# Kernel tuning notes

Measured on AMD Instinct MI355X. Metric: run time of the kernel, lower is better.

The kernel has to match this reference:

```python
import jax, jax.numpy as jnp
import numpy as np
import math

ALPHA = 1.3
N_ITER = 50


def entmax_bisect(logits, alpha=ALPHA, n_iter=N_ITER):
    # logits: [..., D]; entmax over the last axis via bisection on tau.
    x = logits / max(1.0, abs(alpha - 1.0))  # divisor is 1.0 for alpha=1.3
    x = x - jnp.max(x, axis=-1, keepdims=True)  # max_x subtraction (differentiable, as in torch)
    xs = jax.lax.stop_gradient(x)  # tau_lo/tau_hi are .detach()'d in the original
    tau_lo = jnp.min(xs, axis=-1, keepdims=True) - 1.0
    tau_hi = jnp.max(xs, axis=-1, keepdims=True) - 1e-6
    inv = 1.0 / (alpha - 1.0)

    def body(_, carry):
        lo, hi = carry
        tau = (lo + hi) * 0.5
        p = jnp.maximum(xs - tau, 0.0) ** inv
        f = jnp.sum(p, axis=-1, keepdims=True) ** (alpha - 1.0)
        big = f > 1.0
        return (jnp.where(big, tau, lo), jnp.where(big, hi, tau))

    tau_lo, tau_hi = jax.lax.fori_loop(0, n_iter, body, (tau_lo, tau_hi))
    tau = (tau_lo + tau_hi) * 0.5
    p = jnp.maximum(x - tau, 0.0) ** inv
    return p / (jnp.sum(p, axis=-1, keepdims=True) + 1e-12)


def setup_inputs() -> dict:
    key = jax.random.key(0)
    kq, kk, kv = jax.random.split(key, 3)
    B, N, D = 16, 2048, 64
    return {
        "q": jax.random.normal(kq, (B, N, D), dtype=jnp.float32),
        "k": jax.random.normal(kk, (B, N, D), dtype=jnp.float32),
        "v": jax.random.normal(kv, (B, N, D), dtype=jnp.float32),
    }


def reference(q, k, v):
    d = q.shape[-1]
    scores = jnp.einsum("bnd,bmd->bnm", q, k) / math.sqrt(d)  # [B,N,N]
    attn = entmax_bisect(scores, alpha=ALPHA)
    out = jnp.einsum("bnm,bmd->bnd", attn, v)
    return out, attn
```

## Files before the change

kernel.cpp:

```cpp
#include <hip/hip_runtime.h>


#define NBATCH 16
#define NSEQ   2048
#define DHEAD  64
#define OUT_OFF (NBATCH * NSEQ * DHEAD)
#define INV_A    3.3333333f
#define INV_A_M1 2.3333333f
#define IDXM 0x7FFu
#define VALM 0xFFFFF800u

typedef float  vfloat4 __attribute__((ext_vector_type(4)));
typedef float  f32x4   __attribute__((ext_vector_type(4)));
typedef short  bf16x8  __attribute__((ext_vector_type(8)));
typedef unsigned short u16x8 __attribute__((ext_vector_type(8)));

__device__ __forceinline__ float fast_log2(float x) { return __builtin_amdgcn_logf(x); }
__device__ __forceinline__ float fast_exp2(float x) { return __builtin_amdgcn_exp2f(x); }

__device__ __forceinline__ unsigned bf16_rne(float x) {
    const unsigned u = __float_as_uint(x);
    return (u + 0x7FFFu + ((u >> 16) & 1u)) >> 16;
}

__global__ __launch_bounds__(256) void ksplit_kernel(
    const float* __restrict__ K, unsigned short* __restrict__ Khi,
    unsigned short* __restrict__ Klo)
{
    const size_t idx = (size_t)blockIdx.x * 256 + threadIdx.x;
    const float4 x = ((const float4*)K)[idx];
    const float xs[4] = {x.x, x.y, x.z, x.w};
    unsigned short h[4], l[4];
    #pragma unroll
    for (int i = 0; i < 4; ++i) {
        const unsigned hr = bf16_rne(xs[i]);
        h[i] = (unsigned short)hr;
        l[i] = (unsigned short)bf16_rne(xs[i] - __uint_as_float(hr << 16));
    }
    ((ushort4*)Khi)[idx] = make_ushort4(h[0], h[1], h[2], h[3]);
    ((ushort4*)Klo)[idx] = make_ushort4(l[0], l[1], l[2], l[3]);
}

__global__ __launch_bounds__(512) void entmax_attn_kernel(
    const float* __restrict__ Q, const float* __restrict__ V,
    float* __restrict__ Out,
    const unsigned short* __restrict__ Khi, const unsigned short* __restrict__ Klo)
{
    __shared__ __align__(16) float reg0[8192];
    __shared__ __align__(16) float cpk[8 * 256];

    const int tid  = threadIdx.x;
    const int w    = tid >> 6;
    const int lane = tid & 63;
    const int arow = lane & 15;
    const int lg   = lane >> 4;

    const int i   = blockIdx.x;
    const int xcd = i & 7;
    const int j2  = i >> 3;
    const int b   = xcd + 8 * (j2 & 1);
    const int rb  = j2 >> 1;
    const int n0  = rb * 16;

    const float* Vb = V + (size_t)b * NSEQ * DHEAD;
    const unsigned short* KhiB = Khi + (size_t)b * NSEQ * DHEAD;
    const unsigned short* KloB = Klo + (size_t)b * NSEQ * DHEAD;
    char* ldsHi = (char*)reg0;
    char* ldsLo = (char*)reg0 + 16384;

    bf16x8 a_hi[2], a_lo[2];
    {
        const float* qrow = Q + ((size_t)b * NSEQ + (size_t)(n0 + arow)) * DHEAD;
        #pragma unroll
        for (int ks = 0; ks < 2; ++ks) {
            const int d0 = ks * 32 + lg * 8;
            const float4 x0 = *(const float4*)(qrow + d0);
            const float4 x1 = *(const float4*)(qrow + d0 + 4);
            const float xs[8] = {x0.x, x0.y, x0.z, x0.w, x1.x, x1.y, x1.z, x1.w};
            #pragma unroll
            for (int e = 0; e < 8; ++e) {
                const float xq = xs[e] * 0.125f;
                const unsigned hr = bf16_rne(xq);
                a_hi[ks][e] = (short)hr;
                a_lo[ks][e] = (short)bf16_rne(xq - __uint_as_float(hr << 16));
            }
        }
    }

    float s[2][32];
    const int kap = 16 * w + arow;

    const int keyA = tid >> 3, cA = tid & 7;
    const int keyB = keyA + 64;
    const size_t gA = (size_t)keyA * DHEAD + cA * 8;
    const size_t gB = (size_t)keyB * DHEAD + cA * 8;
    const int ofA = keyA * 128 + ((cA ^ (keyA & 7)) << 4);
    const int ofB = keyB * 128 + ((cA ^ (keyA & 7)) << 4);

    u16x8 shA = *(const u16x8*)(KhiB + gA), slA = *(const u16x8*)(KloB + gA);
    u16x8 shB = *(const u16x8*)(KhiB + gB), slB = *(const u16x8*)(KloB + gB);

    #pragma unroll
    for (int g = 0; g < 4; ++g) {
        f32x4 acc[4];
        #pragma unroll
        for (int tt = 0; tt < 4; ++tt) acc[tt] = (f32x4){0.f, 0.f, 0.f, 0.f};

        #pragma unroll
        for (int tt = 0; tt < 4; ++tt) {
            const int t = 4 * g + tt;
            __syncthreads();
            *(u16x8*)(ldsHi + ofA) = shA;  *(u16x8*)(ldsLo + ofA) = slA;
            *(u16x8*)(ldsHi + ofB) = shB;  *(u16x8*)(ldsLo + ofB) = slB;
            __syncthreads();

            #pragma unroll
            for (int ks = 0; ks < 2; ++ks) {
                const int loff = kap * 128 + ((((ks << 2) | lg) ^ (kap & 7)) << 4);
                const bf16x8 bh = *(const bf16x8*)(ldsHi + loff);
                const bf16x8 bl = *(const bf16x8*)(ldsLo + loff);
                acc[tt] = __builtin_amdgcn_mfma_f32_16x16x32_bf16(a_hi[ks], bh, acc[tt], 0, 0, 0);
                acc[tt] = __builtin_amdgcn_mfma_f32_16x16x32_bf16(a_hi[ks], bl, acc[tt], 0, 0, 0);
                acc[tt] = __builtin_amdgcn_mfma_f32_16x16x32_bf16(a_lo[ks], bh, acc[tt], 0, 0, 0);
            }
            if (t < 15) {
                const size_t tb = (size_t)(t + 1) * (128 * DHEAD);
                shA = *(const u16x8*)(KhiB + tb + gA);
                slA = *(const u16x8*)(KloB + tb + gA);
                shB = *(const u16x8*)(KhiB + tb + gB);
                slB = *(const u16x8*)(KloB + tb + gB);
            }
        }

        __syncthreads();
        #pragma unroll
        for (int tt = 0; tt < 4; ++tt)
            #pragma unroll
            for (int i2 = 0; i2 < 4; ++i2)
                reg0[(lg * 4 + i2) * 512 + tt * 128 + kap] = acc[tt][i2];
        __syncthreads();
        #pragma unroll
        for (int r = 0; r < 2; ++r)
            #pragma unroll
            for (int jj = 0; jj < 8; ++jj)
                s[r][8 * g + jj] = reg0[(2 * w + r) * 512 + jj * 64 + lane];
    }
    __syncthreads();

    unsigned* pk0 = (unsigned*)(cpk + w * 256);
    unsigned* pk1 = pk0 + 128;
    float* prow = reg0 + w * 1024;
    const unsigned long long lt_mask = (1ull << lane) - 1ull;
    const int na = n0 + 2 * w;

    float mx0 = s[0][0], mx1 = s[1][0];
    #pragma unroll
    for (int j = 1; j < 32; ++j) { mx0 = fmaxf(mx0, s[0][j]); mx1 = fmaxf(mx1, s[1][j]); }
    #pragma unroll
    for (int off = 32; off >= 1; off >>= 1) {
        mx0 = fmaxf(mx0, __shfl_xor(mx0, off, 64));
        mx1 = fmaxf(mx1, __shfl_xor(mx1, off, 64));
    }

    int base0 = 0, base1 = 0;
    #pragma unroll
    for (int j = 0; j < 32; ++j) {
        const float v0 = s[0][j] - mx0;
        const float v1 = s[1][j] - mx1;
        const bool a0 = v0 > -1.0f;
        const bool a1 = v1 > -1.0f;
        const unsigned long long bm0 = __ballot(a0);
        const unsigned long long bm1 = __ballot(a1);
        const int q0 = base0 + __popcll(bm0 & lt_mask);
        const int q1 = base1 + __popcll(bm1 & lt_mask);
        const unsigned idx = (unsigned)(j * 64 + lane);
        if (a0 && q0 < 128) pk0[q0] = (__float_as_uint(v0) & VALM) | idx;
        if (a1 && q1 < 128) pk1[q1] = (__float_as_uint(v1) & VALM) | idx;
        base0 += __popcll(bm0);
        base1 += __popcll(bm1);
    }
    const int A0 = base0, A1 = base1;

    float* arow0 = Out + OUT_OFF + ((size_t)b * NSEQ + na) * NSEQ;
    float* arow1 = arow0 + NSEQ;

    if (A0 <= 128 && A1 <= 128) {
        const unsigned u00 = pk0[lane],      u01 = pk0[64 + lane];
        const unsigned u10 = pk1[lane],      u11 = pk1[64 + lane];
        const float cv00 = __uint_as_float(u00 & VALM);
        const float cv01 = __uint_as_float(u01 & VALM);
        const float cv10 = __uint_as_float(u10 & VALM);
        const float cv11 = __uint_as_float(u11 & VALM);
        const bool ok00 = lane < A0, ok01 = 64 + lane < A0;
        const bool ok10 = lane < A1, ok11 = 64 + lane < A1;

        float lo0 = -1.0f, hi0 = -1e-6f, lo1 = -1.0f, hi1 = -1e-6f;
        #pragma unroll 1
        for (int it = 0; it < 8; ++it) {
            const float ta = 0.5f * (lo0 + hi0);
            const float tb = 0.5f * (lo1 + hi1);
            const float t00 = cv00 - ta, t01 = cv01 - ta;
            const float t10 = cv10 - tb, t11 = cv11 - tb;
            float S0 = ((ok00 && t00 > 0.f) ? fast_exp2(INV_A * fast_log2(t00)) : 0.f)
                     + ((ok01 && t01 > 0.f) ? fast_exp2(INV_A * fast_log2(t01)) : 0.f);
            float S1 = ((ok10 && t10 > 0.f) ? fast_exp2(INV_A * fast_log2(t10)) : 0.f)
                     + ((ok11 && t11 > 0.f) ? fast_exp2(INV_A * fast_log2(t11)) : 0.f);
            #pragma unroll
            for (int off = 32; off >= 1; off >>= 1) {
                S0 += __shfl_xor(S0, off, 64);
                S1 += __shfl_xor(S1, off, 64);
            }
            if (S0 > 1.f) lo0 = ta; else hi0 = ta;
            if (S1 > 1.f) lo1 = tb; else hi1 = tb;
        }
        float tau0 = lo0, tau1 = lo1;
        #pragma unroll 1
        for (int it = 0; it < 2; ++it) {
            const float t00 = cv00 - tau0, t01 = cv01 - tau0;
            const float t10 = cv10 - tau1, t11 = cv11 - tau1;
            float Sa0 = 0.f, Sb0 = 0.f, Sa1 = 0.f, Sb1 = 0.f;
            if (ok00 && t00 > 0.f) { const float l = fast_log2(t00); Sa0 += fast_exp2(INV_A * l); Sb0 += fast_exp2(INV_A_M1 * l); }
            if (ok01 && t01 > 0.f) { const float l = fast_log2(t01); Sa0 += fast_exp2(INV_A * l); Sb0 += fast_exp2(INV_A_M1 * l); }
            if (ok10 && t10 > 0.f) { const float l = fast_log2(t10); Sa1 += fast_exp2(INV_A * l); Sb1 += fast_exp2(INV_A_M1 * l); }
            if (ok11 && t11 > 0.f) { const float l = fast_log2(t11); Sa1 += fast_exp2(INV_A * l); Sb1 += fast_exp2(INV_A_M1 * l); }
            #pragma unroll
            for (int off = 32; off >= 1; off >>= 1) {
                Sa0 += __shfl_xor(Sa0, off, 64); Sb0 += __shfl_xor(Sb0, off, 64);
                Sa1 += __shfl_xor(Sa1, off, 64); Sb1 += __shfl_xor(Sb1, off, 64);
            }
            tau0 += (Sa0 - 1.f) / (INV_A * Sb0);
            tau0 = fmaxf(fminf(tau0, hi0), lo0);
            tau1 += (Sa1 - 1.f) / (INV_A * Sb1);
            tau1 = fmaxf(fminf(tau1, hi1), lo1);
        }

        const float t00 = cv00 - tau0, t01 = cv01 - tau0;
        const float t10 = cv10 - tau1, t11 = cv11 - tau1;
        float p00 = (ok00 && t00 > 0.f) ? fast_exp2(INV_A * fast_log2(t00)) : 0.f;
        float p01 = (ok01 && t01 > 0.f) ? fast_exp2(INV_A * fast_log2(t01)) : 0.f;
        float p10 = (ok10 && t10 > 0.f) ? fast_exp2(INV_A * fast_log2(t10)) : 0.f;
        float p11 = (ok11 && t11 > 0.f) ? fast_exp2(INV_A * fast_log2(t11)) : 0.f;
        float S0 = p00 + p01, S1 = p10 + p11;
        #pragma unroll
        for (int off = 32; off >= 1; off >>= 1) {
            S0 += __shfl_xor(S0, off, 64);
            S1 += __shfl_xor(S1, off, 64);
        }
        const float rn0 = 1.f / (S0 + 1e-12f);
        const float rn1 = 1.f / (S1 + 1e-12f);
        p00 *= rn0; p01 *= rn0; p10 *= rn1; p11 *= rn1;
        const int i00 = ok00 ? (int)(u00 & IDXM) : -1;
        const int i01 = ok01 ? (int)(u01 & IDXM) : -1;
        const int i10 = ok10 ? (int)(u10 & IDXM) : -1;
        const int i11 = ok11 ? (int)(u11 & IDXM) : -1;
        if (ok00) pk0[lane]      = (__float_as_uint(p00) & VALM) | (unsigned)i00;
        if (ok01) pk0[64 + lane] = (__float_as_uint(p01) & VALM) | (unsigned)i01;
        if (ok10) pk1[lane]      = (__float_as_uint(p10) & VALM) | (unsigned)i10;
        if (ok11) pk1[64 + lane] = (__float_as_uint(p11) & VALM) | (unsigned)i11;

        #pragma unroll
        for (int seg = 0; seg < 2; ++seg) {
            #pragma unroll
            for (int z = 0; z < 4; ++z)
                *(float4*)&prow[(z * 64 + lane) * 4] = make_float4(0.f, 0.f, 0.f, 0.f);
            if (ok00 && (i00 >> 10) == seg) prow[i00 & 1023] = p00;
            if (ok01 && (i01 >> 10) == seg) prow[i01 & 1023] = p01;
            #pragma unroll
            for (int z = 0; z < 4; ++z) {
                const vfloat4 pv = *(const vfloat4*)&prow[(z * 64 + lane) * 4];
                __builtin_nontemporal_store(pv,
                    (vfloat4*)&arow0[seg * 1024 + (z * 64 + lane) * 4]);
            }
        }
        #pragma unroll
        for (int seg = 0; seg < 2; ++seg) {
            #pragma unroll
            for (int z = 0; z < 4; ++z)
                *(float4*)&prow[(z * 64 + lane) * 4] = make_float4(0.f, 0.f, 0.f, 0.f);
            if (ok10 && (i10 >> 10) == seg) prow[i10 & 1023] = p10;
            if (ok11 && (i11 >> 10) == seg) prow[i11 & 1023] = p11;
            #pragma unroll
            for (int z = 0; z < 4; ++z) {
                const vfloat4 pv = *(const vfloat4*)&prow[(z * 64 + lane) * 4];
                __builtin_nontemporal_store(pv,
                    (vfloat4*)&arow1[seg * 1024 + (z * 64 + lane) * 4]);
            }
        }

        float out0 = 0.f, out1 = 0.f;
        int ii = 0;
        #pragma unroll 1
        for (; ii + 8 <= A0; ii += 8) {
            const unsigned ua = pk0[ii+0], ub = pk0[ii+1], uc = pk0[ii+2], ud = pk0[ii+3];
            const unsigned ue = pk0[ii+4], uf = pk0[ii+5], ug = pk0[ii+6], uh = pk0[ii+7];
            out0 += __uint_as_float(ua & VALM) * Vb[(size_t)(ua & IDXM) * DHEAD + lane]
                  + __uint_as_float(ub & VALM) * Vb[(size_t)(ub & IDXM) * DHEAD + lane]
                  + __uint_as_float(uc & VALM) * Vb[(size_t)(uc & IDXM) * DHEAD + lane]
                  + __uint_as_float(ud & VALM) * Vb[(size_t)(ud & IDXM) * DHEAD + lane]
                  + __uint_as_float(ue & VALM) * Vb[(size_t)(ue & IDXM) * DHEAD + lane]
                  + __uint_as_float(uf & VALM) * Vb[(size_t)(uf & IDXM) * DHEAD + lane]
                  + __uint_as_float(ug & VALM) * Vb[(size_t)(ug & IDXM) * DHEAD + lane]
                  + __uint_as_float(uh & VALM) * Vb[(size_t)(uh & IDXM) * DHEAD + lane];
        }
        #pragma unroll 1
        for (; ii < A0; ++ii) {
            const unsigned ua = pk0[ii];
            out0 += __uint_as_float(ua & VALM) * Vb[(size_t)(ua & IDXM) * DHEAD + lane];
        }
        int jj = 0;
        #pragma unroll 1
        for (; jj + 8 <= A1; jj += 8) {
            const unsigned ua = pk1[jj+0], ub = pk1[jj+1], uc = pk1[jj+2], ud = pk1[jj+3];
            const unsigned ue = pk1[jj+4], uf = pk1[jj+5], ug = pk1[jj+6], uh = pk1[jj+7];
            out1 += __uint_as_float(ua & VALM) * Vb[(size_t)(ua & IDXM) * DHEAD + lane]
                  + __uint_as_float(ub & VALM) * Vb[(size_t)(ub & IDXM) * DHEAD + lane]
                  + __uint_as_float(uc & VALM) * Vb[(size_t)(uc & IDXM) * DHEAD + lane]
                  + __uint_as_float(ud & VALM) * Vb[(size_t)(ud & IDXM) * DHEAD + lane]
                  + __uint_as_float(ue & VALM) * Vb[(size_t)(ue & IDXM) * DHEAD + lane]
                  + __uint_as_float(uf & VALM) * Vb[(size_t)(uf & IDXM) * DHEAD + lane]
                  + __uint_as_float(ug & VALM) * Vb[(size_t)(ug & IDXM) * DHEAD + lane]
                  + __uint_as_float(uh & VALM) * Vb[(size_t)(uh & IDXM) * DHEAD + lane];
        }
        #pragma unroll 1
        for (; jj < A1; ++jj) {
            const unsigned ua = pk1[jj];
            out1 += __uint_as_float(ua & VALM) * Vb[(size_t)(ua & IDXM) * DHEAD + lane];
        }

        Out[((size_t)b * NSEQ + na) * DHEAD + lane] = out0;
        Out[((size_t)b * NSEQ + na + 1) * DHEAD + lane] = out1;
    } else {
        #pragma unroll
        for (int r = 0; r < 2; ++r) {
            const int A = r ? A1 : A0;
            const float mxr = r ? mx1 : mx0;
            unsigned* pk = r ? pk1 : pk0;
            float* arowX = r ? arow1 : arow0;
            float outacc = 0.f;

            if (A <= 128) {
                const unsigned u0 = pk[lane], u1 = pk[64 + lane];
                const float cv0 = __uint_as_float(u0 & VALM);
                const float cv1 = __uint_as_float(u1 & VALM);
                const bool ok0 = (lane < A);
                const bool ok1 = (64 + lane < A);

                float lo = -1.0f, hi = -1e-6f;
                #pragma unroll 1
                for (int it = 0; it < 10; ++it) {
                    const float tau = 0.5f * (lo + hi);
                    const float t0 = cv0 - tau, t1 = cv1 - tau;
                    float S = ((ok0 && t0 > 0.f) ? fast_exp2(INV_A * fast_log2(t0)) : 0.f)
                            + ((ok1 && t1 > 0.f) ? fast_exp2(INV_A * fast_log2(t1)) : 0.f);
                    #pragma unroll
                    for (int off = 32; off >= 1; off >>= 1) S += __shfl_xor(S, off, 64);
                    if (S > 1.f) lo = tau; else hi = tau;
                }
                float tau = lo;
                #pragma unroll 1
                for (int it = 0; it < 2; ++it) {
                    const float t0 = cv0 - tau, t1 = cv1 - tau;
                    float S1 = 0.f, S2 = 0.f;
                    if (ok0 && t0 > 0.f) { const float l = fast_log2(t0); S1 += fast_exp2(INV_A * l); S2 += fast_exp2(INV_A_M1 * l); }
                    if (ok1 && t1 > 0.f) { const float l = fast_log2(t1); S1 += fast_exp2(INV_A * l); S2 += fast_exp2(INV_A_M1 * l); }
                    #pragma unroll
                    for (int off = 32; off >= 1; off >>= 1) {
                        S1 += __shfl_xor(S1, off, 64);
                        S2 += __shfl_xor(S2, off, 64);
                    }
                    tau += (S1 - 1.f) / (INV_A * S2);
                    tau = fmaxf(fminf(tau, hi), lo);
                }
                const float t0 = cv0 - tau, t1 = cv1 - tau;
                float p0 = (ok0 && t0 > 0.f) ? fast_exp2(INV_A * fast_log2(t0)) : 0.f;
                float p1 = (ok1 && t1 > 0.f) ? fast_exp2(INV_A * fast_log2(t1)) : 0.f;
                float S = p0 + p1;
                #pragma unroll
                for (int off = 32; off >= 1; off >>= 1) S += __shfl_xor(S, off, 64);
                const float rnorm = 1.f / (S + 1e-12f);
                p0 *= rnorm; p1 *= rnorm;
                const int i0 = ok0 ? (int)(u0 & IDXM) : -1;
                const int i1 = ok1 ? (int)(u1 & IDXM) : -1;
                if (ok0) pk[lane]      = (__float_as_uint(p0) & VALM) | (unsigned)i0;
                if (ok1) pk[64 + lane] = (__float_as_uint(p1) & VALM) | (unsigned)i1;

                #pragma unroll
                for (int seg = 0; seg < 2; ++seg) {
                    #pragma unroll
                    for (int z = 0; z < 4; ++z)
                        *(float4*)&prow[(z * 64 + lane) * 4] = make_float4(0.f, 0.f, 0.f, 0.f);
                    if (ok0 && (i0 >> 10) == seg) prow[i0 & 1023] = p0;
                    if (ok1 && (i1 >> 10) == seg) prow[i1 & 1023] = p1;
                    #pragma unroll
                    for (int z = 0; z < 4; ++z) {
                        const vfloat4 pv = *(const vfloat4*)&prow[(z * 64 + lane) * 4];
                        __builtin_nontemporal_store(pv,
                            (vfloat4*)&arowX[seg * 1024 + (z * 64 + lane) * 4]);
                    }
                }

                int ii = 0;
                #pragma unroll 1
                for (; ii + 4 <= A; ii += 4) {
                    const unsigned ua = pk[ii+0], ub = pk[ii+1], uc = pk[ii+2], ud = pk[ii+3];
                    outacc += __uint_as_float(ua & VALM) * Vb[(size_t)(ua & IDXM) * DHEAD + lane]
                            + __uint_as_float(ub & VALM) * Vb[(size_t)(ub & IDXM) * DHEAD + lane]
                            + __uint_as_float(uc & VALM) * Vb[(size_t)(uc & IDXM) * DHEAD + lane]
                            + __uint_as_float(ud & VALM) * Vb[(size_t)(ud & IDXM) * DHEAD + lane];
                }
                #pragma unroll 1
                for (; ii < A; ++ii) {
                    const unsigned ua = pk[ii];
                    outacc += __uint_as_float(ua & VALM) * Vb[(size_t)(ua & IDXM) * DHEAD + lane];
                }
            } else {
                float lo = -1.0f, hi = -1e-6f;
                #pragma unroll 1
                for (int it = 0; it < 12; ++it) {
                    const float tau = 0.5f * (lo + hi);
                    float S = 0.f;
                    #pragma unroll
                    for (int j = 0; j < 32; ++j) {
                        const float t = s[r][j] - mxr - tau;
                        const float p = fast_exp2(INV_A * fast_log2(t));
                        S += (t > 0.f) ? p : 0.f;
                    }
                    #pragma unroll
                    for (int off = 32; off >= 1; off >>= 1) S += __shfl_xor(S, off, 64);
                    if (S > 1.f) lo = tau; else hi = tau;
                }
                float tau = lo;
                #pragma unroll 1
                for (int it = 0; it < 2; ++it) {
                    float S1 = 0.f, S2 = 0.f;
                    #pragma unroll
                    for (int j = 0; j < 32; ++j) {
                        const float t = s[r][j] - mxr - tau;
                        if (t > 0.f) {
                            const float l = fast_log2(t);
                            S1 += fast_exp2(INV_A * l); S2 += fast_exp2(INV_A_M1 * l);
                        }
                    }
                    #pragma unroll
                    for (int off = 32; off >= 1; off >>= 1) {
                        S1 += __shfl_xor(S1, off, 64);
                        S2 += __shfl_xor(S2, off, 64);
                    }
                    tau += (S1 - 1.f) / (INV_A * S2);
                    tau = fmaxf(fminf(tau, hi), lo);
                }
                float S = 0.f;
                #pragma unroll
                for (int j = 0; j < 32; ++j) {
                    const float t = s[r][j] - mxr - tau;
                    const float p = (t > 0.f) ? fast_exp2(INV_A * fast_log2(t)) : 0.f;
                    s[r][j] = p;
                    S += p;
                }
                #pragma unroll
                for (int off = 32; off >= 1; off >>= 1) S += __shfl_xor(S, off, 64);
                const float rnorm = 1.f / (S + 1e-12f);

                #pragma unroll
                for (int seg = 0; seg < 2; ++seg) {
                    #pragma unroll
                    for (int jj = 0; jj < 16; ++jj)
                        prow[jj * 64 + lane] = s[r][seg * 16 + jj] * rnorm;
                    #pragma unroll
                    for (int z = 0; z < 16; ++z)
                        __builtin_nontemporal_store(prow[z * 64 + lane],
                                                    &arowX[seg * 1024 + z * 64 + lane]);
                    #pragma unroll 4
                    for (int m = 0; m < 1024; ++m)
                        outacc += prow[m] * Vb[(size_t)(seg * 1024 + m) * DHEAD + lane];
                }
            }

            Out[((size_t)b * NSEQ + (na + r)) * DHEAD + lane] = outacc;
        }
    }
}

extern "C" void kernel_launch(void* const* d_in, const int* in_sizes, int n_in,
                              void* d_out, int out_size, void* d_ws, size_t ws_size,
                              hipStream_t stream) {
    const float* q = (const float*)d_in[0];
    const float* k = (const float*)d_in[1];
    const float* v = (const float*)d_in[2];
    float* out = (float*)d_out;
    (void)in_sizes; (void)n_in; (void)out_size; (void)ws_size;

    unsigned short* Khi = (unsigned short*)d_ws;
    unsigned short* Klo = Khi + (size_t)NBATCH * NSEQ * DHEAD;

    hipLaunchKernelGGL(ksplit_kernel, dim3(2048), dim3(256), 0, stream, k, Khi, Klo);
    hipLaunchKernelGGL(entmax_attn_kernel, dim3(2048), dim3(512), 0, stream,
                       q, v, out, Khi, Klo);
}
```

Measured before the change: 482.2 us.

## Zero attention rows early and scatter sparse probabilities directly to global

Attention rows are zero-filled with nontemporal vector stores before the entmax computation, so their write traffic can overlap the bisection work. The sparse nonzero probabilities are then scattered straight to global memory after an explicit vmcnt wait, replacing the LDS staging buffer that zeroed, filled and re-read each row segment. The dense fallback path now writes probabilities directly and broadcasts them with shuffles for the PV product instead of reading them back from LDS. The change relies on the zero stores finishing before the scattered stores, which the inline vmcnt wait is meant to guarantee, and the dense path's per-element shuffles may cost more than the LDS reads they replace.

Result: slower. 655.6 us (+36.0%).

```diff
diff --git a/kernel.cpp b/kernel.cpp
--- a/kernel.cpp
+++ b/kernel.cpp
@@ -149,9 +149,21 @@
 
     unsigned* pk0 = (unsigned*)(cpk + w * 256);
     unsigned* pk1 = pk0 + 128;
-    float* prow = reg0 + w * 1024;
     const unsigned long long lt_mask = (1ull << lane) - 1ull;
     const int na = n0 + 2 * w;
+
+    float* arow0 = Out + OUT_OFF + ((size_t)b * NSEQ + na) * NSEQ;
+    float* arow1 = arow0 + NSEQ;
+
+    {
+        const vfloat4 z4 = (vfloat4){0.f, 0.f, 0.f, 0.f};
+        #pragma unroll
+        for (int z = 0; z < 8; ++z)
+            __builtin_nontemporal_store(z4, (vfloat4*)&arow0[(z * 64 + lane) * 4]);
+        #pragma unroll
+        for (int z = 0; z < 8; ++z)
+            __builtin_nontemporal_store(z4, (vfloat4*)&arow1[(z * 64 + lane) * 4]);
+    }
 
     float mx0 = s[0][0], mx1 = s[1][0];
     #pragma unroll
@@ -181,9 +193,6 @@
     }
     const int A0 = base0, A1 = base1;
 
-    float* arow0 = Out + OUT_OFF + ((size_t)b * NSEQ + na) * NSEQ;
-    float* arow1 = arow0 + NSEQ;
-
     if (A0 <= 128 && A1 <= 128) {
         const unsigned u00 = pk0[lane],      u01 = pk0[64 + lane];
         const unsigned u10 = pk1[lane],      u11 = pk1[64 + lane];
@@ -258,34 +267,11 @@
         if (ok10) pk1[lane]      = (__float_as_uint(p10) & VALM) | (unsigned)i10;
         if (ok11) pk1[64 + lane] = (__float_as_uint(p11) & VALM) | (unsigned)i11;
 
-        #pragma unroll
-        for (int seg = 0; seg < 2; ++seg) {
-            #pragma unroll
-            for (int z = 0; z < 4; ++z)
-                *(float4*)&prow[(z * 64 + lane) * 4] = make_float4(0.f, 0.f, 0.f, 0.f);
-            if (ok00 && (i00 >> 10) == seg) prow[i00 & 1023] = p00;
-            if (ok01 && (i01 >> 10) == seg) prow[i01 & 1023] = p01;
-            #pragma unroll
-            for (int z = 0; z < 4; ++z) {
-                const vfloat4 pv = *(const vfloat4*)&prow[(z * 64 + lane) * 4];
-                __builtin_nontemporal_store(pv,
-                    (vfloat4*)&arow0[seg * 1024 + (z * 64 + lane) * 4]);
-            }
-        }
-        #pragma unroll
-        for (int seg = 0; seg < 2; ++seg) {
-            #pragma unroll
-            for (int z = 0; z < 4; ++z)
-                *(float4*)&prow[(z * 64 + lane) * 4] = make_float4(0.f, 0.f, 0.f, 0.f);
-            if (ok10 && (i10 >> 10) == seg) prow[i10 & 1023] = p10;
-            if (ok11 && (i11 >> 10) == seg) prow[i11 & 1023] = p11;
-            #pragma unroll
-            for (int z = 0; z < 4; ++z) {
-                const vfloat4 pv = *(const vfloat4*)&prow[(z * 64 + lane) * 4];
-                __builtin_nontemporal_store(pv,
-                    (vfloat4*)&arow1[seg * 1024 + (z * 64 + lane) * 4]);
-            }
-        }
+        asm volatile("s_waitcnt vmcnt(0)" ::: "memory");
+        if (ok00) arow0[i00] = p00;
+        if (ok01) arow0[i01] = p01;
+        if (ok10) arow1[i10] = p10;
+        if (ok11) arow1[i11] = p11;
 
         float out0 = 0.f, out1 = 0.f;
         int ii = 0;
@@ -384,20 +370,9 @@
                 if (ok0) pk[lane]      = (__float_as_uint(p0) & VALM) | (unsigned)i0;
                 if (ok1) pk[64 + lane] = (__float_as_uint(p1) & VALM) | (unsigned)i1;
 
-                #pragma unroll
-                for (int seg = 0; seg < 2; ++seg) {
-                    #pragma unroll
-                    for (int z = 0; z < 4; ++z)
-                        *(float4*)&prow[(z * 64 + lane) * 4] = make_float4(0.f, 0.f, 0.f, 0.f);
-                    if (ok0 && (i0 >> 10) == seg) prow[i0 & 1023] = p0;
-                    if (ok1 && (i1 >> 10) == seg) prow[i1 & 1023] = p1;
-                    #pragma unroll
-                    for (int z = 0; z < 4; ++z) {
-                        const vfloat4 pv = *(const vfloat4*)&prow[(z * 64 + lane) * 4];
-                        __builtin_nontemporal_store(pv,
-                            (vfloat4*)&arowX[seg * 1024 + (z * 64 + lane) * 4]);
-                    }
-                }
+                asm volatile("s_waitcnt vmcnt(0)" ::: "memory");
+                if (ok0) arowX[i0] = p0;
+                if (ok1) arowX[i1] = p1;
 
                 int ii = 0;
                 #pragma unroll 1
@@ -461,18 +436,16 @@
                 for (int off = 32; off >= 1; off >>= 1) S += __shfl_xor(S, off, 64);
                 const float rnorm = 1.f / (S + 1e-12f);
 
+                asm volatile("s_waitcnt vmcnt(0)" ::: "memory");
                 #pragma unroll
-                for (int seg = 0; seg < 2; ++seg) {
-                    #pragma unroll
-                    for (int jj = 0; jj < 16; ++jj)
-                        prow[jj * 64 + lane] = s[r][seg * 16 + jj] * rnorm;
-                    #pragma unroll
-                    for (int z = 0; z < 16; ++z)
-                        __builtin_nontemporal_store(prow[z * 64 + lane],
-                                                    &arowX[seg * 1024 + z * 64 + lane]);
-                    #pragma unroll 4
-                    for (int m = 0; m < 1024; ++m)
-                        outacc += prow[m] * Vb[(size_t)(seg * 1024 + m) * DHEAD + lane];
+                for (int j = 0; j < 32; ++j) {
+                    const float pj = s[r][j] * rnorm;
+                    arowX[j * 64 + lane] = pj;
+                    #pragma unroll 1
+                    for (int l = 0; l < 64; ++l) {
+                        const float pv = __shfl(pj, l, 64);
+                        outacc += pv * Vb[(size_t)(j * 64 + l) * DHEAD + lane];
+                    }
                 }
             }
 
```
